# Optimization experiments

Measured on AMD Instinct MI355X. Metric: run time of the kernel, lower is better.

## Reference

```python
import jax, jax.numpy as jnp
import numpy as np
from jax import lax

D_MODEL, D_INNER, D_STATE, D_CONV, DT_RANK = 1024, 2048, 16, 4, 64
B, L = 1, 2048


def setup_inputs() -> dict:
    key = jax.random.key(0)
    ks = jax.random.split(key, 10)
    s = lambda d: 1.0 / np.sqrt(d)
    return {
        "x": jax.random.normal(ks[0], (B, L, D_MODEL), jnp.float32),
        "W_in": jax.random.normal(ks[1], (D_MODEL, 2 * D_INNER), jnp.float32) * s(D_MODEL),
        "conv_w": jax.random.normal(ks[2], (D_INNER, D_CONV), jnp.float32) * s(D_CONV),
        "conv_b": jax.random.normal(ks[3], (D_INNER,), jnp.float32) * 0.01,
        "W_x": jax.random.normal(ks[4], (D_INNER, DT_RANK + 2 * D_STATE), jnp.float32) * s(D_INNER),
        "W_dt": jax.random.normal(ks[5], (DT_RANK, D_INNER), jnp.float32) * s(DT_RANK),
        "b_dt": jax.random.normal(ks[6], (D_INNER,), jnp.float32) * 0.01,
        # A = arange(1, d_state+1) repeated over d_inner; A_log = log(A)
        "A_log": jnp.log(jnp.tile(jnp.arange(1.0, D_STATE + 1.0, dtype=jnp.float32), (D_INNER, 1))),
        "D": jnp.ones((D_INNER,), jnp.float32),
        "W_out": jax.random.normal(ks[7], (D_INNER, D_MODEL), jnp.float32) * s(D_INNER),
    }


def reference(x, W_in, conv_w, conv_b, W_x, W_dt, b_dt, A_log, D, W_out):
    b, l, dm = x.shape
    di, n = A_log.shape[0], A_log.shape[1]
    # input projection + split into conv branch and gate residual
    x_and_res = x @ W_in                          # (b, l, 2*di)
    xc, res = x_and_res[..., :di], x_and_res[..., di:]
    # causal depthwise conv1d (left pad k-1, matches torch padding=k-1 + slice[:l])
    k = conv_w.shape[1]
    xp = jnp.pad(xc, ((0, 0), (k - 1, 0), (0, 0)))
    xconv = conv_b
    for j in range(k):
        xconv = xconv + xp[:, j:j + l, :] * conv_w[:, j]
    xs = jax.nn.silu(xconv)                       # (b, l, di)
    # selection parameters
    x_dbl = xs @ W_x                              # (b, l, dt_rank + 2n)
    dt_r = x_dbl[..., :DT_RANK]
    Bm = x_dbl[..., DT_RANK:DT_RANK + n]          # (b, l, n)
    Cm = x_dbl[..., DT_RANK + n:]                 # (b, l, n)
    dt = jax.nn.softplus(dt_r @ W_dt + b_dt)      # (b, l, di)
    A = -jnp.exp(A_log)                           # (di, n)
    # discretize
    dA = jnp.exp(jnp.einsum('bld,dn->bldn', dt, A))
    dBx = jnp.einsum('bld,bln->bldn', dt, Bm) * xs[..., None]
    # sequential state scan over time
    def step(h, inp):
        dA_t, dBx_t, C_t = inp                    # (b,di,n),(b,di,n),(b,n)
        h = dA_t * h + dBx_t
        y = jnp.einsum('bdn,bn->bd', h, C_t)
        return h, y
    h0 = jnp.zeros((b, di, n), x.dtype)
    hT, ys = lax.scan(step, h0, (dA.transpose(1, 0, 2, 3),
                                 dBx.transpose(1, 0, 2, 3),
                                 Cm.transpose(1, 0, 2)))
    y = ys.transpose(1, 0, 2) + xs * D            # (b, l, di)
    y = y * jax.nn.silu(res)
    out = y @ W_out                               # (b, l, d_model)
    return out, hT
```

## Files before the change

### kernel.cpp

```cpp
#include <hip/hip_runtime.h>
#include <math.h>

#define DM 1024
#define DI 2048
#define NS 16
#define DTR 64
#define LL 2048
#define NXDBL 96
#define NCHUNK 128
#define CHLEN 16

typedef unsigned short u16;
typedef __attribute__((ext_vector_type(8))) short short8;
typedef __attribute__((ext_vector_type(4))) float f32x4;

__device__ __forceinline__ float sigmoidf_(float x) { return 1.f / (1.f + __expf(-x)); }
__device__ __forceinline__ float siluf_(float x) { return x * sigmoidf_(x); }
__device__ __forceinline__ float softplus_fast(float x) {
    return fmaxf(x, 0.f) + __logf(1.f + __expf(-fabsf(x)));
}
__device__ __forceinline__ u16 f2b(float f) {
    unsigned u = __float_as_uint(f);
    return (u16)((u + 0x7FFFu + ((u >> 16) & 1u)) >> 16);
}

__device__ __forceinline__ void convT_dev(const float* __restrict__ src,
                                          u16* __restrict__ dst, int R, int C,
                                          int bflat, int gridx, float (*t)[33]) {
    const int tx = threadIdx.x & 31, ty = threadIdx.x >> 5;
    const int c0 = (bflat % gridx) * 32, r0 = (bflat / gridx) * 32;
#pragma unroll
    for (int i = 0; i < 4; i++)
        t[ty + i * 8][tx] = src[(size_t)(r0 + ty + i * 8) * C + c0 + tx];
    __syncthreads();
#pragma unroll
    for (int i = 0; i < 4; i++)
        dst[(size_t)(c0 + ty + i * 8) * R + r0 + tx] = f2b(t[tx][ty + i * 8]);
}

#define PREP_BLOCKS 8640
__global__ __launch_bounds__(256) void prep_all(const float* __restrict__ x,
                                                u16* __restrict__ xb,
                                                const float* __restrict__ W_in,
                                                u16* __restrict__ W_inT,
                                                const float* __restrict__ W_out,
                                                u16* __restrict__ W_outT,
                                                const float* __restrict__ W_x,
                                                u16* __restrict__ W_xT_pad) {
    __shared__ float t[32][33];
    const int b = blockIdx.x;
    if (b < 2048) {
        const int i = (b * 256 + threadIdx.x) * 4;
        float4 v = *(const float4*)&x[i];
        u16 o[4] = {f2b(v.x), f2b(v.y), f2b(v.z), f2b(v.w)};
        *(ushort4*)&xb[i] = *(ushort4*)o;
    } else if (b < 6144) {
        convT_dev(W_in, W_inT, DM, 2 * DI, b - 2048, 2 * DI / 32, t);
    } else if (b < 8192) {
        convT_dev(W_out, W_outT, DI, DM, b - 6144, DM / 32, t);
    } else if (b < 8384) {
        convT_dev(W_x, W_xT_pad, DI, NXDBL, b - 8192, NXDBL / 32, t);
    } else {
        const int i = (b - 8384) * 256 + threadIdx.x;
        if (i < 32 * DI) W_xT_pad[96 * DI + i] = 0;
    }
}

#define WAITV(N) asm volatile("s_waitcnt vmcnt(" #N ")" ::: "memory")
template <int EPI, int NSTEPS>
__global__ __launch_bounds__(256) void gemm_mfma(const u16* __restrict__ A,
                                                 const u16* __restrict__ Bt,
                                                 float* __restrict__ C0,
                                                 float* __restrict__ C1,
                                                 int M, int N, int lda) {
    __shared__ u16 As[3][128 * 32];
    __shared__ u16 Bs[3][128 * 32];
    const int tid = threadIdx.x;
    const int lane = tid & 63;
    const int wave = tid >> 6;
    const int bm = blockIdx.y * 128, bn = blockIdx.x * 128;
    const int wr = wave >> 1, wc = wave & 1;
    const int k_off = blockIdx.z * (NSTEPS * 32);

    f32x4 acc[4][4];
#pragma unroll
    for (int m = 0; m < 4; m++)
#pragma unroll
        for (int n = 0; n < 4; n++) acc[m][n] = (f32x4)0.f;

    const int srow = tid >> 2;
    const int swz = (tid >> 3) & 3;
    const int skel = (((tid & 3) ^ swz) << 3);
    const u16* Ag0 = A + (size_t)(bm + srow) * lda + k_off + skel;
    const u16* Ag1 = A + (size_t)(bm + 64 + srow) * lda + k_off + skel;
    const u16* Bg0 = Bt + (size_t)(bn + srow) * lda + k_off + skel;
    const u16* Bg1 = Bt + (size_t)(bn + 64 + srow) * lda + k_off + skel;
    u16* Asl = &As[0][0] + tid * 8;
    u16* Bsl = &Bs[0][0] + tid * 8;

    const int rsw = (lane >> 1) & 3;
    const int arow = (wr * 64 + (lane & 15)) * 32 + (((lane >> 4) ^ rsw) << 3);
    const int brow = (wc * 64 + (lane & 15)) * 32 + (((lane >> 4) ^ rsw) << 3);

#define STAGE(buf, ks)                                                               \
    do {                                                                             \
        __builtin_amdgcn_global_load_lds(                                            \
            (const __attribute__((address_space(1))) unsigned*)(Ag0 + (ks)),         \
            (__attribute__((address_space(3))) unsigned*)(Asl + (buf) * 4096),       \
            16, 0, 0);                                                               \
        __builtin_amdgcn_global_load_lds(                                            \
            (const __attribute__((address_space(1))) unsigned*)(Ag1 + (ks)),         \
            (__attribute__((address_space(3))) unsigned*)(Asl + (buf) * 4096 + 2048),\
            16, 0, 0);                                                               \
        __builtin_amdgcn_global_load_lds(                                            \
            (const __attribute__((address_space(1))) unsigned*)(Bg0 + (ks)),         \
            (__attribute__((address_space(3))) unsigned*)(Bsl + (buf) * 4096),       \
            16, 0, 0);                                                               \
        __builtin_amdgcn_global_load_lds(                                            \
            (const __attribute__((address_space(1))) unsigned*)(Bg1 + (ks)),         \
            (__attribute__((address_space(3))) unsigned*)(Bsl + (buf) * 4096 + 2048),\
            16, 0, 0);                                                               \
    } while (0)

#define COMPUTE(buf)                                                                 \
    do {                                                                             \
        short8 av[4], bv[4];                                                         \
        _Pragma("unroll") for (int m = 0; m < 4; m++)                                \
            av[m] = *(const short8*)&As[buf][arow + m * 512];                        \
        _Pragma("unroll") for (int n = 0; n < 4; n++)                                \
            bv[n] = *(const short8*)&Bs[buf][brow + n * 512];                        \
        _Pragma("unroll") for (int m = 0; m < 4; m++)                                \
            _Pragma("unroll") for (int n = 0; n < 4; n++)                            \
                acc[m][n] = __builtin_amdgcn_mfma_f32_16x16x32_bf16(av[m], bv[n],    \
                                                                    acc[m][n], 0, 0, 0); \
    } while (0)

    STAGE(0, 0);
    if (NSTEPS > 1) STAGE(1, 32);
#pragma unroll
    for (int s = 0; s < NSTEPS; ++s) {
        if (s + 2 < NSTEPS) {
            STAGE((s + 2) % 3, (s + 2) * 32);
            WAITV(8);
        } else if (s + 1 < NSTEPS) {
            WAITV(4);
        } else {
            WAITV(0);
        }
        __builtin_amdgcn_s_barrier();
        COMPUTE(s % 3);
        __builtin_amdgcn_s_barrier();
    }
#undef STAGE
#undef COMPUTE

    const int crow0 = bm + wr * 64 + (lane >> 4) * 4;
    const int ccol0 = bn + wc * 64 + (lane & 15);
    float* C0z = C0 + (size_t)blockIdx.z * M * N;
#pragma unroll
    for (int m = 0; m < 4; m++)
#pragma unroll
        for (int n = 0; n < 4; n++) {
            const int col = ccol0 + n * 16;
#pragma unroll
            for (int r = 0; r < 4; r++) {
                const int row = crow0 + m * 16 + r;
                const float v = acc[m][n][r];
                if (EPI == 1) {
                    if (col < DI)
                        C0[(size_t)row * DI + col] = v;
                    else
                        C1[(size_t)row * DI + col - DI] = v;
                } else {
                    C0z[(size_t)row * N + col] = v;
                }
            }
        }
}

__global__ __launch_bounds__(256) void gemm128_dt(const float* __restrict__ A,
                                                  const float* __restrict__ B,
                                                  const float* __restrict__ bias,
                                                  float* __restrict__ C,
                                                  int N, int K, int lda) {
    __shared__ float As[16][128];
    __shared__ float Bs[16][128];
    const int tid = threadIdx.x;
    const int bm = blockIdx.y * 128, bn = blockIdx.x * 128;
    const int ty = tid >> 4, tx = tid & 15;
    float acc[8][8];
#pragma unroll
    for (int i = 0; i < 8; i++)
#pragma unroll
        for (int j = 0; j < 8; j++) acc[i][j] = 0.f;

    const int ar = tid >> 2, ak = (tid & 3) << 2;
    const int bk = tid >> 5, bc = (tid & 31) << 2;

    for (int k0 = 0; k0 < K; k0 += 16) {
        float4 a0 = *(const float4*)&A[(size_t)(bm + ar) * lda + k0 + ak];
        float4 a1 = *(const float4*)&A[(size_t)(bm + ar + 64) * lda + k0 + ak];
        float4 b0 = *(const float4*)&B[(size_t)(k0 + bk) * N + bn + bc];
        float4 b1 = *(const float4*)&B[(size_t)(k0 + bk + 8) * N + bn + bc];
        __syncthreads();
        As[ak + 0][ar] = a0.x; As[ak + 1][ar] = a0.y;
        As[ak + 2][ar] = a0.z; As[ak + 3][ar] = a0.w;
        As[ak + 0][ar + 64] = a1.x; As[ak + 1][ar + 64] = a1.y;
        As[ak + 2][ar + 64] = a1.z; As[ak + 3][ar + 64] = a1.w;
        *(float4*)&Bs[bk][bc] = b0;
        *(float4*)&Bs[bk + 8][bc] = b1;
        __syncthreads();
#pragma unroll
        for (int k = 0; k < 16; k++) {
            float a[8], b[8];
            *(float4*)&a[0] = *(const float4*)&As[k][ty * 8];
            *(float4*)&a[4] = *(const float4*)&As[k][ty * 8 + 4];
            *(float4*)&b[0] = *(const float4*)&Bs[k][tx * 8];
            *(float4*)&b[4] = *(const float4*)&Bs[k][tx * 8 + 4];
#pragma unroll
            for (int i = 0; i < 8; i++)
#pragma unroll
                for (int j = 0; j < 8; j++) acc[i][j] = fmaf(a[i], b[j], acc[i][j]);
        }
    }
#pragma unroll
    for (int i = 0; i < 8; i++) {
        const int row = bm + ty * 8 + i;
#pragma unroll
        for (int j = 0; j < 8; j += 4) {
            const int col = bn + tx * 8 + j;
            const float4 bi = *(const float4*)&bias[col];
            float4 v = make_float4(softplus_fast(acc[i][j] + bi.x),
                                   softplus_fast(acc[i][j + 1] + bi.y),
                                   softplus_fast(acc[i][j + 2] + bi.z),
                                   softplus_fast(acc[i][j + 3] + bi.w));
            *(float4*)&C[(size_t)row * N + col] = v;
        }
    }
}

__global__ __launch_bounds__(256) void sum4(const float* __restrict__ p,
                                            float* __restrict__ out, int n) {
    const int i = (blockIdx.x * 256 + threadIdx.x) * 4;
    float4 a = *(const float4*)&p[i];
    float4 b = *(const float4*)&p[(size_t)n + i];
    float4 c = *(const float4*)&p[2 * (size_t)n + i];
    float4 d = *(const float4*)&p[3 * (size_t)n + i];
    *(float4*)&out[i] = make_float4((a.x + b.x) + (c.x + d.x),
                                    (a.y + b.y) + (c.y + d.y),
                                    (a.z + b.z) + (c.z + d.z),
                                    (a.w + b.w) + (c.w + d.w));
}

__global__ __launch_bounds__(256) void g2reduce(const float* __restrict__ part,
                                                float* __restrict__ xdbl) {
    const int gid = blockIdx.x * 256 + threadIdx.x;
    if (gid < LL * NXDBL) {
        const int row = gid / NXDBL;
        const int col = gid - row * NXDBL;
        float s = 0.f;
#pragma unroll
        for (int z = 0; z < 16; z++) s += part[((size_t)z * LL + row) * 128 + col];
        xdbl[gid] = s;
    }
}

__global__ __launch_bounds__(256) void conv_silu(const float* __restrict__ xc,
                                                 const float* __restrict__ cw,
                                                 const float* __restrict__ cb,
                                                 float* __restrict__ xs,
                                                 u16* __restrict__ xsb) {
    const int gid = blockIdx.x * 256 + threadIdx.x;
    const int l = gid >> 11;
    const int d = gid & (DI - 1);
    const float4 w = *(const float4*)&cw[d * 4];
    float acc = cb[d];
    const float wj[4] = {w.x, w.y, w.z, w.w};
#pragma unroll
    for (int j = 0; j < 4; j++) {
        const int li = l + j - 3;
        if (li >= 0) acc = fmaf(xc[(size_t)li * DI + d], wj[j], acc);
    }
    const float s = siluf_(acc);
    xs[gid] = s;
    xsb[gid] = f2b(s);
}

__global__ __launch_bounds__(256) void scan_phase1(const float* __restrict__ dt,
                                                   const float* __restrict__ xs,
                                                   const float* __restrict__ xdbl,
                                                   const float* __restrict__ A_log,
                                                   float* __restrict__ chA,
                                                   float* __restrict__ chB) {
    const int g = blockIdx.x * 256 + threadIdx.x;
    const int d = g & (DI - 1);
    const int c = g >> 11;
    float An2[NS], ap[NS], bc[NS];
    {
        float al[NS];
#pragma unroll
        for (int q = 0; q < 4; q++)
            *(float4*)&al[q * 4] = *(const float4*)&A_log[d * NS + q * 4];
#pragma unroll
        for (int n = 0; n < NS; n++) {
            An2[n] = -__expf(al[n]) * 1.44269504f;
            ap[n] = 1.f;
            bc[n] = 0.f;
        }
    }
    const int l0 = c * CHLEN;
    for (int l = l0; l < l0 + CHLEN; ++l) {
        const float dtv = dt[(size_t)l * DI + d];
        const float xsv = xs[(size_t)l * DI + d];
        const float dx = dtv * xsv;
        float bv[NS];
#pragma unroll
        for (int q = 0; q < 4; q++)
            *(float4*)&bv[q * 4] = *(const float4*)&xdbl[(size_t)l * NXDBL + DTR + q * 4];
#pragma unroll
        for (int n = 0; n < NS; n++) {
            const float al = __builtin_amdgcn_exp2f(dtv * An2[n]);
            ap[n] *= al;
            bc[n] = fmaf(al, bc[n], dx * bv[n]);
        }
    }
    const size_t o = ((size_t)c * DI + d) * NS;
#pragma unroll
    for (int q = 0; q < 4; q++) {
        *(float4*)&chA[o + q * 4] = *(float4*)&ap[q * 4];
        *(float4*)&chB[o + q * 4] = *(float4*)&bc[q * 4];
    }
}

__global__ __launch_bounds__(256) void scan_phase2(float* __restrict__ chA,
                                                   const float* __restrict__ chB,
                                                   float* __restrict__ hT_out) {
    const int t = blockIdx.x * 256 + threadIdx.x;
    float h = 0.f;
#pragma unroll 4
    for (int c = 0; c < NCHUNK; ++c) {
        const size_t o = (size_t)c * DI * NS + t;
        const float a = chA[o];
        const float b = chB[o];
        chA[o] = h;
        h = fmaf(a, h, b);
    }
    hT_out[t] = h;
}

__global__ __launch_bounds__(256) void scan_phase3(const float* __restrict__ dt,
                                                   const float* __restrict__ xs,
                                                   const float* __restrict__ xdbl,
                                                   const float* __restrict__ A_log,
                                                   const float* __restrict__ h0,
                                                   const float* __restrict__ Dw,
                                                   const float* __restrict__ res,
                                                   u16* __restrict__ yb) {
    const int g = blockIdx.x * 256 + threadIdx.x;
    const int d = g & (DI - 1);
    const int c = g >> 11;
    float An2[NS], h[NS];
    {
        float al[NS];
#pragma unroll
        for (int q = 0; q < 4; q++)
            *(float4*)&al[q * 4] = *(const float4*)&A_log[d * NS + q * 4];
#pragma unroll
        for (int n = 0; n < NS; n++) An2[n] = -__expf(al[n]) * 1.44269504f;
    }
    const size_t ho = ((size_t)c * DI + d) * NS;
#pragma unroll
    for (int q = 0; q < 4; q++) *(float4*)&h[q * 4] = *(const float4*)&h0[ho + q * 4];
    const float Dd = Dw[d];
    const int l0 = c * CHLEN;
    for (int l = l0; l < l0 + CHLEN; ++l) {
        const float dtv = dt[(size_t)l * DI + d];
        const float xsv = xs[(size_t)l * DI + d];
        const float resv = res[(size_t)l * DI + d];
        const float dx = dtv * xsv;
        float bv[NS], cv[NS];
#pragma unroll
        for (int q = 0; q < 4; q++) {
            *(float4*)&bv[q * 4] = *(const float4*)&xdbl[(size_t)l * NXDBL + DTR + q * 4];
            *(float4*)&cv[q * 4] =
                *(const float4*)&xdbl[(size_t)l * NXDBL + DTR + NS + q * 4];
        }
#pragma unroll
        for (int n = 0; n < NS; n++) {
            const float al = __builtin_amdgcn_exp2f(dtv * An2[n]);
            h[n] = fmaf(al, h[n], dx * bv[n]);
        }
        float y0 = 0.f, y1 = 0.f, y2 = 0.f, y3 = 0.f;
#pragma unroll
        for (int n = 0; n < NS; n += 4) {
            y0 = fmaf(h[n + 0], cv[n + 0], y0);
            y1 = fmaf(h[n + 1], cv[n + 1], y1);
            y2 = fmaf(h[n + 2], cv[n + 2], y2);
            y3 = fmaf(h[n + 3], cv[n + 3], y3);
        }
        float yv = ((y0 + y1) + (y2 + y3)) + xsv * Dd;
        yv *= siluf_(resv);
        yb[(size_t)l * DI + d] = f2b(yv);
    }
}

extern "C" void kernel_launch(void* const* d_in, const int* in_sizes, int n_in,
                              void* d_out, int out_size, void* d_ws, size_t ws_size,
                              hipStream_t stream) {
    const float* x = (const float*)d_in[0];
    const float* W_in = (const float*)d_in[1];
    const float* conv_w = (const float*)d_in[2];
    const float* conv_b = (const float*)d_in[3];
    const float* W_x = (const float*)d_in[4];
    const float* W_dt = (const float*)d_in[5];
    const float* b_dt = (const float*)d_in[6];
    const float* A_log = (const float*)d_in[7];
    const float* Dw = (const float*)d_in[8];
    const float* W_out = (const float*)d_in[9];
    float* out = (float*)d_out;

    float* ws = (float*)d_ws;
    float* xc       = ws;
    float* res      = ws + 4194304;
    float* xs       = ws + 8388608;
    float* dt       = ws + 12582912;
    float* xdbl     = ws + 16777216;
    float* chA      = ws + 16973824;
    float* chB      = ws + 21168128;
    u16*   xb       = (u16*)(ws + 25362432);
    u16*   W_inT_b  = (u16*)(ws + 26411008);
    u16*   W_outT_b = (u16*)(ws + 28508160);
    u16*   xs_b     = (u16*)(ws + 29556736);
    u16*   W_xT_pad = (u16*)(ws + 31653888);
    float* g2part   = ws + 31784960;
    float* g4part   = ws + 35979264;
    u16*   yb       = (u16*)(ws + 44367872);

    prep_all<<<PREP_BLOCKS, 256, 0, stream>>>(x, xb, W_in, W_inT_b, W_out, W_outT_b,
                                              W_x, W_xT_pad);
    gemm_mfma<1, DM / 32><<<dim3(2 * DI / 128, LL / 128), 256, 0, stream>>>(
        xb, W_inT_b, xc, res, LL, 2 * DI, DM);
    conv_silu<<<(LL * DI) / 256, 256, 0, stream>>>(xc, conv_w, conv_b, xs, xs_b);
    gemm_mfma<0, 4><<<dim3(1, LL / 128, 16), 256, 0, stream>>>(
        xs_b, W_xT_pad, g2part, nullptr, LL, 128, DI);
    g2reduce<<<(LL * NXDBL + 255) / 256, 256, 0, stream>>>(g2part, xdbl);
    gemm128_dt<<<dim3(DI / 128, LL / 128), 256, 0, stream>>>(xdbl, W_dt, b_dt, dt,
                                                             DI, DTR, NXDBL);
    scan_phase1<<<(DI * NCHUNK) / 256, 256, 0, stream>>>(dt, xs, xdbl, A_log, chA, chB);
    scan_phase2<<<(DI * NS) / 256, 256, 0, stream>>>(chA, chB, out + (size_t)LL * DM);
    scan_phase3<<<(DI * NCHUNK) / 256, 256, 0, stream>>>(dt, xs, xdbl, A_log, chA, Dw,
                                                         res, yb);
    gemm_mfma<0, DI / 128><<<dim3(DM / 128, LL / 128, 4), 256, 0, stream>>>(
        yb, W_outT_b, g4part, nullptr, LL, DM, DI);
    sum4<<<(LL * DM) / 1024, 256, 0, stream>>>(g4part, out, LL * DM);
}
```

Before: 171.7 us.

## Store conv branch in bf16, compact x_dbl partials, and remap GEMM tile order

The input-projection GEMM now writes the conv branch xc as bf16 instead of fp32, and conv_silu reads it back as bf16. This halves the write and read traffic for that 2048x2048 intermediate, at the cost of rounding xc to bf16 before the convolution. The x_dbl split-K partials are stored compacted to 96 columns, so g2reduce reads contiguous memory. GEMM blocks are also remapped so each group of eight consecutive block IDs walks column-major across tiles, which is meant to improve L2/MALL locality, and the scan_phase2 unroll is raised from 4 to 16.

```diff
diff --git a/kernel.cpp b/kernel.cpp
--- a/kernel.cpp
+++ b/kernel.cpp
@@ -22,6 +22,9 @@
 __device__ __forceinline__ u16 f2b(float f) {
     unsigned u = __float_as_uint(f);
     return (u16)((u + 0x7FFFu + ((u >> 16) & 1u)) >> 16);
+}
+__device__ __forceinline__ float b2f(u16 h) {
+    return __uint_as_float(((unsigned)h) << 16);
 }
 
 __device__ __forceinline__ void convT_dev(const float* __restrict__ src,
@@ -70,15 +73,19 @@
 template <int EPI, int NSTEPS>
 __global__ __launch_bounds__(256) void gemm_mfma(const u16* __restrict__ A,
                                                  const u16* __restrict__ Bt,
-                                                 float* __restrict__ C0,
-                                                 float* __restrict__ C1,
-                                                 int M, int N, int lda) {
+                                                 void* __restrict__ C0,
+                                                 void* __restrict__ C1,
+                                                 int M, int N, int lda, int nreal) {
     __shared__ u16 As[3][128 * 32];
     __shared__ u16 Bs[3][128 * 32];
     const int tid = threadIdx.x;
     const int lane = tid & 63;
     const int wave = tid >> 6;
-    const int bm = blockIdx.y * 128, bn = blockIdx.x * 128;
+    const int gx = gridDim.x, gy = gridDim.y;
+    const int nb = gx * gy;
+    const int h = blockIdx.y * gx + blockIdx.x;
+    const int f = (h & 7) * (nb >> 3) + (h >> 3);
+    const int bm = (f % gy) * 128, bn = (f / gy) * 128;
     const int wr = wave >> 1, wc = wave & 1;
     const int k_off = blockIdx.z * (NSTEPS * 32);
 
@@ -156,7 +163,6 @@
 
     const int crow0 = bm + wr * 64 + (lane >> 4) * 4;
     const int ccol0 = bn + wc * 64 + (lane & 15);
-    float* C0z = C0 + (size_t)blockIdx.z * M * N;
 #pragma unroll
     for (int m = 0; m < 4; m++)
 #pragma unroll
@@ -168,11 +174,12 @@
                 const float v = acc[m][n][r];
                 if (EPI == 1) {
                     if (col < DI)
-                        C0[(size_t)row * DI + col] = v;
+                        ((u16*)C0)[(size_t)row * DI + col] = f2b(v);
                     else
-                        C1[(size_t)row * DI + col - DI] = v;
+                        ((float*)C1)[(size_t)row * DI + col - DI] = v;
                 } else {
-                    C0z[(size_t)row * N + col] = v;
+                    float* C0z = (float*)C0 + (size_t)blockIdx.z * M * nreal;
+                    if (col < nreal) C0z[(size_t)row * nreal + col] = v;
                 }
             }
         }
@@ -256,16 +263,14 @@
                                                 float* __restrict__ xdbl) {
     const int gid = blockIdx.x * 256 + threadIdx.x;
     if (gid < LL * NXDBL) {
-        const int row = gid / NXDBL;
-        const int col = gid - row * NXDBL;
         float s = 0.f;
 #pragma unroll
-        for (int z = 0; z < 16; z++) s += part[((size_t)z * LL + row) * 128 + col];
+        for (int z = 0; z < 16; z++) s += part[(size_t)z * LL * NXDBL + gid];
         xdbl[gid] = s;
     }
 }
 
-__global__ __launch_bounds__(256) void conv_silu(const float* __restrict__ xc,
+__global__ __launch_bounds__(256) void conv_silu(const u16* __restrict__ xcb,
                                                  const float* __restrict__ cw,
                                                  const float* __restrict__ cb,
                                                  float* __restrict__ xs,
@@ -279,7 +284,7 @@
 #pragma unroll
     for (int j = 0; j < 4; j++) {
         const int li = l + j - 3;
-        if (li >= 0) acc = fmaf(xc[(size_t)li * DI + d], wj[j], acc);
+        if (li >= 0) acc = fmaf(b2f(xcb[(size_t)li * DI + d]), wj[j], acc);
     }
     const float s = siluf_(acc);
     xs[gid] = s;
@@ -337,7 +342,7 @@
                                                    float* __restrict__ hT_out) {
     const int t = blockIdx.x * 256 + threadIdx.x;
     float h = 0.f;
-#pragma unroll 4
+#pragma unroll 16
     for (int c = 0; c < NCHUNK; ++c) {
         const size_t o = (size_t)c * DI * NS + t;
         const float a = chA[o];
@@ -420,7 +425,7 @@
     float* out = (float*)d_out;
 
     float* ws = (float*)d_ws;
-    float* xc       = ws;
+    u16*   xcb      = (u16*)ws;
     float* res      = ws + 4194304;
     float* xs       = ws + 8388608;
     float* dt       = ws + 12582912;
@@ -439,10 +444,10 @@
     prep_all<<<PREP_BLOCKS, 256, 0, stream>>>(x, xb, W_in, W_inT_b, W_out, W_outT_b,
                                               W_x, W_xT_pad);
     gemm_mfma<1, DM / 32><<<dim3(2 * DI / 128, LL / 128), 256, 0, stream>>>(
-        xb, W_inT_b, xc, res, LL, 2 * DI, DM);
-    conv_silu<<<(LL * DI) / 256, 256, 0, stream>>>(xc, conv_w, conv_b, xs, xs_b);
+        xb, W_inT_b, xcb, res, LL, 2 * DI, DM, 2 * DI);
+    conv_silu<<<(LL * DI) / 256, 256, 0, stream>>>(xcb, conv_w, conv_b, xs, xs_b);
     gemm_mfma<0, 4><<<dim3(1, LL / 128, 16), 256, 0, stream>>>(
-        xs_b, W_xT_pad, g2part, nullptr, LL, 128, DI);
+        xs_b, W_xT_pad, g2part, nullptr, LL, 128, DI, NXDBL);
     g2reduce<<<(LL * NXDBL + 255) / 256, 256, 0, stream>>>(g2part, xdbl);
     gemm128_dt<<<dim3(DI / 128, LL / 128), 256, 0, stream>>>(xdbl, W_dt, b_dt, dt,
                                                              DI, DTR, NXDBL);
@@ -451,6 +456,6 @@
     scan_phase3<<<(DI * NCHUNK) / 256, 256, 0, stream>>>(dt, xs, xdbl, A_log, chA, Dw,
                                                          res, yb);
     gemm_mfma<0, DI / 128><<<dim3(DM / 128, LL / 128, 4), 256, 0, stream>>>(
-        yb, W_outT_b, g4part, nullptr, LL, DM, DI);
+        yb, W_outT_b, g4part, nullptr, LL, DM, DI, DM);
     sum4<<<(LL * DM) / 1024, 256, 0, stream>>>(g4part, out, LL * DM);
 }
```

New measurement: 165.0 us. 3.9% less time.
